# Kernel tuning notes

Hardware: AMD Instinct MI355X
Metric: run time of the kernel (lower is better)

## Reference

```python
import jax, jax.numpy as jnp
import numpy as np

# Model dims
D = 2048        # hidden_size
H = 16          # num_heads
KVH = 8         # num_key_value_heads
DH = 128        # head_dim
NUM_SLOTS = 16  # state-cache slots
B = 4           # prefill segments (regularized ragged batch)
L = 2048        # tokens per segment
T = B * L
C = 64          # GLA chunk size (fused_chunk_gla)
NEG = -1e30


def setup_inputs() -> dict:
    key = jax.random.key(0)
    k0, k1, k2, k3 = jax.random.split(key, 4)
    hidden_states = jax.random.normal(k0, (T, D), jnp.float32)
    W_qkv = jax.random.normal(k1, (D, (H + 2 * KVH) * DH), jnp.float32) * 0.02
    b_qkv = jnp.zeros(((H + 2 * KVH) * DH,), jnp.float32)
    kv_cache = jax.random.normal(k2, (NUM_SLOTS, H, DH, DH), jnp.float32) * 0.1
    state_indices = jax.random.randint(k3, (B,), 0, NUM_SLOTS, jnp.int32)
    return {"hidden_states": hidden_states, "W_qkv": W_qkv, "b_qkv": b_qkv,
            "kv_cache": kv_cache, "state_indices": state_indices}


def _to_chunks(x):
    # [T, H, d] -> [n_chunks, B, C, H, d]
    return x.reshape(B, L // C, C, H, DH).transpose(1, 0, 2, 3, 4)


def _gla_chunk_body(mask):
    def body(S, inp):
        # S: [B,H,dk,dv]; qc/kc/vc/gc: [B,C,H,d]
        qc, kc, vc, gc = inp
        Bc = jnp.cumsum(gc, axis=1)                       # inclusive log-decay within chunk
        # inter-chunk: initial state decayed by exp(Bc)
        o_inter = jnp.einsum('bchk,bhkv->bchv', qc * jnp.exp(Bc), S)
        # intra-chunk causal scores: A_ij = sum_d q_i,d * exp(B_i - B_j)_d * k_j,d, j<=i
        diff = Bc[:, :, None] - Bc[:, None, :]            # [B,Ci,Cj,H,dk], <=0 on lower tri
        diff = jnp.where(mask[None, :, :, None, None], diff, NEG)
        A = jnp.einsum('bihk,bijhk,bjhk->bijh', qc, jnp.exp(diff), kc)
        o = o_inter + jnp.einsum('bijh,bjhv->bihv', A, vc)
        # state update: S' = diag(exp(B_last)) S + sum_j (k_j exp(B_last - B_j)) v_j^T
        b_last = Bc[:, -1]                                # [B,H,dk]
        kg = kc * jnp.exp(b_last[:, None] - Bc)
        S_new = S * jnp.exp(b_last)[..., None] + jnp.einsum('bchk,bchv->bhkv', kg, vc)
        return S_new, o
    return jax.checkpoint(body)


def _forward(hidden_states, W_qkv, b_qkv, kv_cache, state_indices):
    qkv = hidden_states @ W_qkv + b_qkv
    q = qkv[:, :H * DH].reshape(T, H, DH)
    k = qkv[:, H * DH:(H + KVH) * DH].reshape(T, KVH, DH)
    v = qkv[:, (H + KVH) * DH:].reshape(T, KVH, DH)
    n_rep = H // KVH
    k = jnp.repeat(k, n_rep, axis=1)                      # repeat_kv (3D branch)
    v = jnp.repeat(v, n_rep, axis=1)
    q = jax.nn.relu(q) * DH ** -0.5                       # q_feature_map + fused_chunk_gla scale
    k = jnp.minimum(jax.nn.sigmoid(k), 0.95)              # sigmoid + clamp(max=clamp_max)
    g = jnp.log1p(-k)                                     # (1 - k).log()

    S0 = kv_cache[state_indices]                          # [B,H,dk,dv] per-slot initial states
    mask = jnp.tril(jnp.ones((C, C), bool))
    _, o = jax.lax.scan(_gla_chunk_body(mask), S0,
                        (_to_chunks(q), _to_chunks(k), _to_chunks(v), _to_chunks(g)))
    # [n_chunks,B,C,H,dv] -> per-segment concat [T, H*dv]
    return o.transpose(1, 0, 2, 3, 4).reshape(T, H * DH)


def reference(hidden_states, W_qkv, b_qkv, kv_cache, state_indices):
    return _forward(hidden_states, W_qkv, b_qkv, kv_cache, state_indices)
```

## Files before the change

### kernel.cpp

```cpp
#include <hip/hip_runtime.h>
#include <hip/hip_bf16.h>
#include <math.h>

#define RSQRT_DH 0.08838834764831845f

typedef __attribute__((ext_vector_type(8))) short short8;
typedef __attribute__((ext_vector_type(4))) float floatx4;

#define BAR() do { asm volatile("" ::: "memory"); __builtin_amdgcn_s_barrier(); asm volatile("" ::: "memory"); } while (0)

static __device__ __forceinline__ float bf2f(unsigned short u) {
  return __uint_as_float(((unsigned int)u) << 16);
}
static __device__ __forceinline__ unsigned short f2bf(float f) {
  unsigned int x = __float_as_uint(f);
  return (unsigned short)((x + 0x7fffu + ((x >> 16) & 1u)) >> 16);
}
static __device__ __forceinline__ ushort4 f4bf(float a, float b, float c, float d) {
  ushort4 r; r.x = f2bf(a); r.y = f2bf(b); r.z = f2bf(c); r.w = f2bf(d); return r;
}
static __device__ __forceinline__ short8 ld8u(const unsigned short* p) {
  short4 a = *(const short4*)p;
  short4 b = *(const short4*)(p + 4);
  short8 r;
  r[0] = a.x; r[1] = a.y; r[2] = a.z; r[3] = a.w;
  r[4] = b.x; r[5] = b.y; r[6] = b.z; r[7] = b.w;
  return r;
}

__launch_bounds__(256)
__global__ void k_cvt(const float* __restrict__ in, unsigned short* __restrict__ out, int n4) {
  int i = blockIdx.x * 256 + threadIdx.x;
  if (i >= n4) return;
  float4 v = ((const float4*)in)[i];
  ((ushort4*)out)[i] = f4bf(v.x, v.y, v.z, v.w);
}

__launch_bounds__(256)
__global__ void k_cvt_wt(const float* __restrict__ W, unsigned short* __restrict__ Wt) {
  __shared__ float tile[32][33];
  int t = threadIdx.x;
  int c = t & 31, r = t >> 5;
  int bx = blockIdx.x, by = blockIdx.y;
#pragma unroll
  for (int j = 0; j < 4; ++j)
    tile[r + j * 8][c] = W[(size_t)(by * 32 + r + j * 8) * 4096 + bx * 32 + c];
  __syncthreads();
#pragma unroll
  for (int j = 0; j < 4; ++j)
    Wt[(size_t)(bx * 32 + r + j * 8) * 2048 + by * 32 + c] = f2bf(tile[c][r + j * 8]);
}

__launch_bounds__(512, 2)
__global__ void k_gemm(const unsigned short* __restrict__ A,
                       const unsigned short* __restrict__ Bt,
                       const float* __restrict__ bias,
                       unsigned short* __restrict__ qb,
                       unsigned short* __restrict__ kb,
                       unsigned short* __restrict__ vb,
                       float* __restrict__ gf) {
  __shared__ unsigned short lds[65536];

  const int tid = threadIdx.x;
  const int w = tid >> 6, l = tid & 63;
  const int wm = w >> 2, wn = w & 3;
  const int lr = l & 15, quad = l >> 4;

  const int id = blockIdx.x;
  const int x = id & 7, loc = id >> 3;
  const int bm = (x >> 1) * 8 + (loc >> 3);
  const int bn = (x & 1) * 8 + (loc & 7);
  const int m0 = bm * 256, n0 = bn * 256;

  const int srow = tid >> 2;
  const int scol = (((tid & 3) ^ ((tid >> 3) & 3)) << 3);
  const unsigned short* agp = A + (size_t)(m0 + srow) * 2048 + scol;
  const unsigned short* bgp = Bt + (size_t)(n0 + srow) * 2048 + scol;
  unsigned short* ldsA_dst = lds + w * 512;
  unsigned short* ldsB_dst = lds + 8192 + w * 512;

  auto stageA = [&](int d, int u, int ktile) {
    __builtin_amdgcn_global_load_lds(
        (const __attribute__((address_space(1))) void*)(agp + (size_t)u * 262144 + (size_t)ktile * 32),
        (__attribute__((address_space(3))) void*)(ldsA_dst + d * 16384 + u * 4096),
        16, 0, 0);
  };
  auto stageB = [&](int d, int u, int ktile) {
    __builtin_amdgcn_global_load_lds(
        (const __attribute__((address_space(1))) void*)(bgp + (size_t)u * 262144 + (size_t)ktile * 32),
        (__attribute__((address_space(3))) void*)(ldsB_dst + d * 16384 + u * 4096),
        16, 0, 0);
  };

  const int kcol = ((quad ^ ((lr >> 1) & 3)) << 3);
  const int arow_base = (wm * 128 + lr) * 32 + kcol;
  const int brow_base = (wn * 64 + lr) * 32 + kcol;

  floatx4 acc[8][4] = {};

#pragma unroll
  for (int pt = 0; pt < 3; ++pt) {
    stageA(pt, 0, pt); stageA(pt, 1, pt);
    stageB(pt, 0, pt); stageB(pt, 1, pt);
  }

  for (int t = 0; t < 64; ++t) {
    const int d = t & 3;
    const unsigned short* Ab = lds + d * 16384;
    const unsigned short* Bb = Ab + 8192;
    const int t3 = t + 3;
    const int d3 = t3 & 3;

    if (t < 62)       asm volatile("s_waitcnt vmcnt(8)" ::: "memory");
    else if (t == 62) asm volatile("s_waitcnt vmcnt(4)" ::: "memory");
    else              asm volatile("s_waitcnt vmcnt(0)" ::: "memory");
    BAR();

    short8 af[4], bfr[4];
#pragma unroll
    for (int i = 0; i < 4; ++i) af[i] = *(const short8*)(Ab + arow_base + i * 512);
#pragma unroll
    for (int i = 0; i < 4; ++i) bfr[i] = *(const short8*)(Bb + brow_base + i * 512);
    if (t3 < 64) { stageA(d3, 0, t3); stageA(d3, 1, t3); }
    __builtin_amdgcn_s_setprio(1);
#pragma unroll
    for (int mi = 0; mi < 4; ++mi)
#pragma unroll
      for (int ni = 0; ni < 4; ++ni)
        acc[mi][ni] = __builtin_amdgcn_mfma_f32_16x16x32_bf16(af[mi], bfr[ni], acc[mi][ni], 0, 0, 0);
    __builtin_amdgcn_s_setprio(0);

    BAR();

#pragma unroll
    for (int i = 0; i < 4; ++i) af[i] = *(const short8*)(Ab + arow_base + 2048 + i * 512);
    if (t3 < 64) { stageB(d3, 0, t3); stageB(d3, 1, t3); }
    __builtin_amdgcn_s_setprio(1);
#pragma unroll
    for (int mi = 0; mi < 4; ++mi)
#pragma unroll
      for (int ni = 0; ni < 4; ++ni)
        acc[4 + mi][ni] = __builtin_amdgcn_mfma_f32_16x16x32_bf16(af[mi], bfr[ni], acc[4 + mi][ni], 0, 0, 0);
    __builtin_amdgcn_s_setprio(0);
  }

  float* ldsf = (float*)lds;
  __syncthreads();

  float4 bv;
  {
    const float* bp = bias + n0 + l * 4;
    bv.x = bp[0]; bv.y = bp[1]; bv.z = bp[2]; bv.w = bp[3];
  }

#pragma unroll
  for (int a = 0; a < 8; ++a) {
#pragma unroll
    for (int ni = 0; ni < 4; ++ni)
#pragma unroll
      for (int r = 0; r < 4; ++r)
        ldsf[(wm * 16 + quad * 4 + r) * 268 + wn * 64 + ni * 16 + lr] = acc[a][ni][r];
    __syncthreads();

    const int rbase = m0 + (a >> 2) * 64 + (a & 3) * 16;
#pragma unroll
    for (int it = 0; it < 4; ++it) {
      const int row32 = w * 4 + it;
      const int grow = rbase + (row32 >> 4) * 128 + (row32 & 15);
      float4 f = *(const float4*)&ldsf[row32 * 268 + l * 4];
      f.x += bv.x; f.y += bv.y; f.z += bv.z; f.w += bv.w;
      if (n0 < 2048) {
        *(ushort4*)(qb + (size_t)grow * 2048 + n0 + l * 4) =
            f4bf(fmaxf(f.x, 0.f) * RSQRT_DH, fmaxf(f.y, 0.f) * RSQRT_DH,
                 fmaxf(f.z, 0.f) * RSQRT_DH, fmaxf(f.w, 0.f) * RSQRT_DH);
      } else if (n0 < 3072) {
        float sx = fminf(1.f / (1.f + __expf(-f.x)), 0.95f);
        float sy = fminf(1.f / (1.f + __expf(-f.y)), 0.95f);
        float sz = fminf(1.f / (1.f + __expf(-f.z)), 0.95f);
        float sw = fminf(1.f / (1.f + __expf(-f.w)), 0.95f);
        size_t idx = (size_t)grow * 1024 + (n0 - 2048) + l * 4;
        *(ushort4*)(kb + idx) = f4bf(sx, sy, sz, sw);
        float4 g4; g4.x = log1pf(-sx); g4.y = log1pf(-sy);
        g4.z = log1pf(-sz); g4.w = log1pf(-sw);
        *(float4*)(gf + idx) = g4;
      } else {
        *(ushort4*)(vb + (size_t)grow * 1024 + (n0 - 3072) + l * 4) =
            f4bf(f.x, f.y, f.z, f.w);
      }
    }
    if (a < 7) __syncthreads();
  }
}

__launch_bounds__(256)
__global__ void k_phaseA(const unsigned short* __restrict__ kb,
                         const unsigned short* __restrict__ vb,
                         const float* __restrict__ gf,
                         float* __restrict__ blast,
                         unsigned short* __restrict__ Pb) {
  __shared__ float sBc[64 * 128];
  __shared__ float sKg[64 * 128];
  const int t = threadIdx.x;
  const int chunk = blockIdx.x, chain = blockIdx.y;
  const int b = chain >> 4, h = chain & 15, kvh = h >> 1;
  const int t0 = b * 2048 + chunk * 64;

#pragma unroll
  for (int rep = 0; rep < 8; ++rep) {
    int e = rep * 256 + t;
    int i = e >> 5, d4 = e & 31;
    *(float4*)(sBc + i * 128 + d4 * 4) =
        *(const float4*)(gf + (size_t)(t0 + i) * 1024 + kvh * 128 + d4 * 4);
  }
  __syncthreads();
  if (t < 128) {
    float run = sBc[t];
    for (int i = 1; i < 64; ++i) { run += sBc[i * 128 + t]; sBc[i * 128 + t] = run; }
    blast[((size_t)chain * 32 + chunk) * 128 + t] = run;
  }
  __syncthreads();
#pragma unroll
  for (int rep = 0; rep < 32; ++rep) {
    int e = rep * 256 + t;
    int i = e >> 7, d = e & 127;
    float kk = bf2f(kb[(size_t)(t0 + i) * 1024 + kvh * 128 + d]);
    sKg[e] = kk * __expf(sBc[63 * 128 + d] - sBc[e]);
  }
  __syncthreads();
  const int kq = t >> 3, vq = t & 7;
  const int kd0 = kq * 4, vd0 = vq * 16;
  float acc[4][16] = {};
  const unsigned short* vrow = vb + (size_t)t0 * 1024 + kvh * 128 + vd0;
  for (int i = 0; i < 64; ++i) {
    float4 kg4 = *(const float4*)(sKg + i * 128 + kd0);
    float ka[4] = {kg4.x, kg4.y, kg4.z, kg4.w};
    ushort4 v0 = *(const ushort4*)(vrow + (size_t)i * 1024);
    ushort4 v1 = *(const ushort4*)(vrow + (size_t)i * 1024 + 4);
    ushort4 v2 = *(const ushort4*)(vrow + (size_t)i * 1024 + 8);
    ushort4 v3 = *(const ushort4*)(vrow + (size_t)i * 1024 + 12);
    float vf[16] = {bf2f(v0.x), bf2f(v0.y), bf2f(v0.z), bf2f(v0.w),
                    bf2f(v1.x), bf2f(v1.y), bf2f(v1.z), bf2f(v1.w),
                    bf2f(v2.x), bf2f(v2.y), bf2f(v2.z), bf2f(v2.w),
                    bf2f(v3.x), bf2f(v3.y), bf2f(v3.z), bf2f(v3.w)};
#pragma unroll
    for (int r = 0; r < 4; ++r)
#pragma unroll
      for (int j = 0; j < 16; ++j) acc[r][j] += ka[r] * vf[j];
  }
  size_t pbase = ((size_t)chain * 32 + chunk) * 16384;
#pragma unroll
  for (int r = 0; r < 4; ++r)
#pragma unroll
    for (int j4 = 0; j4 < 4; ++j4)
      *(ushort4*)(Pb + pbase + (size_t)(kd0 + r) * 128 + vd0 + j4 * 4) =
          f4bf(acc[r][j4 * 4], acc[r][j4 * 4 + 1], acc[r][j4 * 4 + 2], acc[r][j4 * 4 + 3]);
}

__launch_bounds__(256)
__global__ void k_scan(const float* __restrict__ kv_cache,
                       const int* __restrict__ sidx,
                       const float* __restrict__ blast,
                       const unsigned short* __restrict__ Pb,
                       unsigned short* __restrict__ Sb) {
  const int t = threadIdx.x;
  const int part = blockIdx.x;
  const int chain = blockIdx.y;
  const int b = chain >> 4, h = chain & 15;
  const int e0 = part * 1024 + t * 4;
  const int kd = e0 >> 7;
  const int slot = sidx[b];
  float4 s = *(const float4*)(kv_cache + ((size_t)slot * 16 + h) * 16384 + e0);
#pragma unroll 1
  for (int c = 0; c < 32; ++c) {
    *(ushort4*)(Sb + ((size_t)c * 64 + chain) * 16384 + e0) = f4bf(s.x, s.y, s.z, s.w);
    float eb = __expf(blast[((size_t)chain * 32 + c) * 128 + kd]);
    ushort4 p = *(const ushort4*)(Pb + ((size_t)chain * 32 + c) * 16384 + e0);
    s.x = s.x * eb + bf2f(p.x);
    s.y = s.y * eb + bf2f(p.y);
    s.z = s.z * eb + bf2f(p.z);
    s.w = s.w * eb + bf2f(p.w);
  }
}

__launch_bounds__(256)
__global__ void k_output(const unsigned short* __restrict__ qb,
                         const unsigned short* __restrict__ kb,
                         const unsigned short* __restrict__ vb,
                         const float* __restrict__ gf,
                         const unsigned short* __restrict__ Sb,
                         float* __restrict__ out) {
  __shared__ float sBc[64 * 128];
  __shared__ unsigned short sR3[11136];
  unsigned short* sA   = sR3;
  unsigned short* sKE  = sR3 + 4608;
  unsigned short* sQE2 = sR3 + 4608 + 4352;
  unsigned short* sQE0 = sR3;
  unsigned short* sSt  = sR3 + 4608;
  unsigned short* sVt  = sR3 + 4608;

  const int t = threadIdx.x;
  const int w = t >> 6, l = t & 63;
  const int lr = l & 15, quad = l >> 4;
  const int chunk = blockIdx.x, chain = blockIdx.y;
  const int b = chain >> 4, h = chain & 15, kvh = h >> 1;
  const int t0 = b * 2048 + chunk * 64;
  const size_t sbase = ((size_t)chunk * 64 + chain) * 16384;

#pragma unroll
  for (int rep = 0; rep < 8; ++rep) {
    int e = rep * 256 + t, i = e >> 5, d4 = e & 31;
    *(float4*)(sBc + i * 128 + d4 * 4) =
        *(const float4*)(gf + (size_t)(t0 + i) * 1024 + kvh * 128 + d4 * 4);
  }
  __syncthreads();
  if (t < 128) {
    float run = sBc[t];
#pragma unroll
    for (int i = 1; i < 64; ++i) { run += sBc[i * 128 + t]; sBc[i * 128 + t] = run; }
  }

  floatx4 o[8];
#pragma unroll
  for (int i = 0; i < 8; ++i) o[i] = 0.f;

#pragma unroll
  for (int kh = 0; kh < 2; ++kh) {
    __syncthreads();
#pragma unroll
    for (int rep = 0; rep < 2; ++rep) {
      int idx = rep * 256 + t;
      int i = idx >> 3, g = idx & 7;
      int k0 = kh * 64 + g * 8;
      short8 q8 = *(const short8*)(qb + (size_t)(t0 + i) * 2048 + h * 128 + k0);
      short8 r;
#pragma unroll
      for (int u = 0; u < 8; ++u)
        r[u] = (short)f2bf(bf2f((unsigned short)q8[u]) * __expf(sBc[i * 128 + k0 + u]));
      *(short8*)(sQE0 + i * 72 + g * 8) = r;
    }
#pragma unroll
    for (int vh = 0; vh < 2; ++vh) {
      __syncthreads();
#pragma unroll
      for (int rep = 0; rep < 2; ++rep) {
        int idx = rep * 256 + t;
        int kl = idx >> 3, g = idx & 7;
        short8 s8 = *(const short8*)(Sb + sbase + (size_t)(kh * 64 + kl) * 128 + vh * 64 + g * 8);
#pragma unroll
        for (int u = 0; u < 8; ++u) sSt[(g * 8 + u) * 76 + kl] = (unsigned short)s8[u];
      }
      __syncthreads();
      short8 af0 = *(const short8*)(sQE0 + (w * 16 + lr) * 72 + quad * 8);
      short8 af1 = *(const short8*)(sQE0 + (w * 16 + lr) * 72 + 32 + quad * 8);
#pragma unroll
      for (int tv = 0; tv < 4; ++tv) {
        const unsigned short* bp = sSt + (tv * 16 + lr) * 76 + quad * 8;
        short8 bf0 = ld8u(bp);
        short8 bf1 = ld8u(bp + 32);
        o[vh * 4 + tv] = __builtin_amdgcn_mfma_f32_16x16x32_bf16(af0, bf0, o[vh * 4 + tv], 0, 0, 0);
        o[vh * 4 + tv] = __builtin_amdgcn_mfma_f32_16x16x32_bf16(af1, bf1, o[vh * 4 + tv], 0, 0, 0);
      }
    }
  }

  __syncthreads();
  for (int idx = t; idx < 576; idx += 256)
    *(short8*)(sA + idx * 8) = (short8)0;
#pragma unroll
  for (int I = 0; I < 4; ++I) {
    const float* Rrow = (I > 0) ? (sBc + (I * 16 - 1) * 128) : nullptr;
    for (int base = 0; base < (I + 1) * 16; base += 32) {
      int nrows = min(32, (I + 1) * 16 - base);
      __syncthreads();
      int ngroups = nrows * 16;
      for (int idx = t; idx < ngroups; idx += 256) {
        int jl = idx >> 4, g = idx & 15;
        int j = base + jl, k0 = g * 8;
        short8 k8 = *(const short8*)(kb + (size_t)(t0 + j) * 1024 + kvh * 128 + k0);
        short8 r;
#pragma unroll
        for (int u = 0; u < 8; ++u) {
          int k = k0 + u;
          float Rk = Rrow ? Rrow[k] : 0.f;
          r[u] = (short)f2bf(bf2f((unsigned short)k8[u]) * __expf(Rk - sBc[j * 128 + k]));
        }
        *(short8*)(sKE + jl * 136 + k0) = r;
      }
      if (base == 0) {
        {
          int idx = t;
          int il = idx >> 4, g = idx & 15;
          int i = I * 16 + il, k0 = g * 8;
          short8 q8 = *(const short8*)(qb + (size_t)(t0 + i) * 2048 + h * 128 + k0);
          short8 r;
#pragma unroll
          for (int u = 0; u < 8; ++u) {
            int k = k0 + u;
            float Rk = Rrow ? Rrow[k] : 0.f;
            r[u] = (short)f2bf(bf2f((unsigned short)q8[u]) * __expf(sBc[i * 128 + k] - Rk));
          }
          *(short8*)(sQE2 + il * 136 + k0) = r;
        }
      }
      __syncthreads();
      const int J = w;
      if (J * 16 >= base && J * 16 < base + nrows) {
        floatx4 a4 = {};
#pragma unroll
        for (int ks = 0; ks < 4; ++ks) {
          short8 afr = *(const short8*)(sQE2 + lr * 136 + ks * 32 + quad * 8);
          short8 bfr = *(const short8*)(sKE + (J * 16 - base + lr) * 136 + ks * 32 + quad * 8);
          a4 = __builtin_amdgcn_mfma_f32_16x16x32_bf16(afr, bfr, a4, 0, 0, 0);
        }
#pragma unroll
        for (int r = 0; r < 4; ++r) {
          int il = quad * 4 + r;
          float v = ((J < I) || (lr <= il)) ? a4[r] : 0.f;
          sA[(I * 16 + il) * 72 + J * 16 + lr] = f2bf(v);
        }
      }
    }
  }

  __syncthreads();
  short8 aA0 = *(const short8*)(sA + (w * 16 + lr) * 72 + quad * 8);
  short8 aA1 = *(const short8*)(sA + (w * 16 + lr) * 72 + 32 + quad * 8);
#pragma unroll
  for (int vh = 0; vh < 2; ++vh) {
    if (vh) __syncthreads();
#pragma unroll
    for (int rep = 0; rep < 2; ++rep) {
      int idx = rep * 256 + t;
      int j = idx >> 3, g = idx & 7;
      short8 v8 = *(const short8*)(vb + (size_t)(t0 + j) * 1024 + kvh * 128 + vh * 64 + g * 8);
#pragma unroll
      for (int u = 0; u < 8; ++u) sVt[(g * 8 + u) * 76 + j] = (unsigned short)v8[u];
    }
    __syncthreads();
#pragma unroll
    for (int tv = 0; tv < 4; ++tv) {
      const unsigned short* bp = sVt + (tv * 16 + lr) * 76 + quad * 8;
      short8 b0 = ld8u(bp);
      short8 b1 = ld8u(bp + 32);
      o[vh * 4 + tv] = __builtin_amdgcn_mfma_f32_16x16x32_bf16(aA0, b0, o[vh * 4 + tv], 0, 0, 0);
      o[vh * 4 + tv] = __builtin_amdgcn_mfma_f32_16x16x32_bf16(aA1, b1, o[vh * 4 + tv], 0, 0, 0);
    }
  }

#pragma unroll
  for (int tv8 = 0; tv8 < 8; ++tv8) {
    int col = (tv8 >> 2) * 64 + (tv8 & 3) * 16 + lr;
#pragma unroll
    for (int r = 0; r < 4; ++r) {
      int i = w * 16 + quad * 4 + r;
      out[(size_t)(t0 + i) * 2048 + h * 128 + col] = o[tv8][r];
    }
  }
}

extern "C" void kernel_launch(void* const* d_in, const int* in_sizes, int n_in,
                              void* d_out, int out_size, void* d_ws, size_t ws_size,
                              hipStream_t stream) {
  (void)in_sizes; (void)n_in; (void)out_size; (void)ws_size;
  const float* hs   = (const float*)d_in[0];
  const float* W    = (const float*)d_in[1];
  const float* bias = (const float*)d_in[2];
  const float* kvc  = (const float*)d_in[3];
  const int*   sidx = (const int*)d_in[4];

  char* ws = (char*)d_ws;
  unsigned short* Sb  = (unsigned short*)(ws + 0);
  unsigned short* hsb = (unsigned short*)(ws + 0);
  unsigned short* wtb = (unsigned short*)(ws + 33554432);
  unsigned short* qb  = (unsigned short*)(ws + 67108864);
  unsigned short* kb  = (unsigned short*)(ws + 100663296);
  unsigned short* vb  = (unsigned short*)(ws + 117440512);
  float*          gf  = (float*)(ws + 134217728);
  float*          bl  = (float*)(ws + 167772160);
  unsigned short* Pb  = (unsigned short*)d_out;
  float* out = (float*)d_out;

  k_cvt<<<dim3(16384), dim3(256), 0, stream>>>(hs, hsb, 16777216 / 4);
  k_cvt_wt<<<dim3(128, 64), dim3(256), 0, stream>>>(W, wtb);
  k_gemm<<<dim3(512), dim3(512), 0, stream>>>(hsb, wtb, bias, qb, kb, vb, gf);
  k_phaseA<<<dim3(32, 64), dim3(256), 0, stream>>>(kb, vb, gf, bl, Pb);
  k_scan<<<dim3(16, 64), dim3(256), 0, stream>>>(kvc, sidx, bl, Pb, Sb);
  k_output<<<dim3(32, 64), dim3(256), 0, stream>>>(qb, kb, vb, gf, Sb, out);
}
```

Measured before the change: 588.9 us.

## Restructure QKV GEMM to double-buffered K=64 tiles and parallelize chunk cumsum

The QKV projection GEMM main loop moves from a 4-stage ring of K=32 tiles to a 2-stage double buffer of K=64 tiles with a new XOR swizzle. Each K tile is split into four MFMA quadrants, with fragment loads and global-to-LDS prefetch interleaved between barriers, so there are fewer loop iterations and more MFMA work per synchronization. Separately, the per-chunk cumulative sum in phaseA and the output kernel becomes a log-step parallel scan over all 256 threads instead of a serial 64-step loop on 128 threads. The tradeoffs are a shallower prefetch depth in the GEMM, more barriers per iteration, and extra LDS traffic and barriers in the scan.

```diff
diff --git a/kernel.cpp b/kernel.cpp
--- a/kernel.cpp
+++ b/kernel.cpp
@@ -8,6 +8,7 @@
 typedef __attribute__((ext_vector_type(4))) float floatx4;
 
 #define BAR() do { asm volatile("" ::: "memory"); __builtin_amdgcn_s_barrier(); asm volatile("" ::: "memory"); } while (0)
+#define MFMA16(a, b, c) __builtin_amdgcn_mfma_f32_16x16x32_bf16((a), (b), (c), 0, 0, 0)
 
 static __device__ __forceinline__ float bf2f(unsigned short u) {
   return __uint_as_float(((unsigned int)u) << 16);
@@ -60,6 +61,7 @@
                        unsigned short* __restrict__ vb,
                        float* __restrict__ gf) {
   __shared__ unsigned short lds[65536];
+  char* lb = (char*)lds;
 
   const int tid = threadIdx.x;
   const int w = tid >> 6, l = tid & 63;
@@ -72,76 +74,118 @@
   const int bn = (x & 1) * 8 + (loc & 7);
   const int m0 = bm * 256, n0 = bn * 256;
 
-  const int srow = tid >> 2;
-  const int scol = (((tid & 3) ^ ((tid >> 3) & 3)) << 3);
-  const unsigned short* agp = A + (size_t)(m0 + srow) * 2048 + scol;
-  const unsigned short* bgp = Bt + (size_t)(n0 + srow) * 2048 + scol;
-  unsigned short* ldsA_dst = lds + w * 512;
-  unsigned short* ldsB_dst = lds + 8192 + w * 512;
-
-  auto stageA = [&](int d, int u, int ktile) {
+  const int srow = tid >> 3;
+  const int sslot = (tid & 7) ^ (srow & 7);
+  const unsigned short* agp = A + (size_t)(m0 + srow) * 2048 + sslot * 8;
+  const unsigned short* bgp = Bt + (size_t)(n0 + srow) * 2048 + sslot * 8;
+
+  auto stA = [&](int d, int h, int s, int kt) {
     __builtin_amdgcn_global_load_lds(
-        (const __attribute__((address_space(1))) void*)(agp + (size_t)u * 262144 + (size_t)ktile * 32),
-        (__attribute__((address_space(3))) void*)(ldsA_dst + d * 16384 + u * 4096),
+        (const __attribute__((address_space(1))) void*)(agp + (size_t)(h * 128 + s * 64) * 2048 + kt * 64),
+        (__attribute__((address_space(3))) void*)(lb + d * 65536 + h * 16384 + s * 8192 + tid * 16),
         16, 0, 0);
   };
-  auto stageB = [&](int d, int u, int ktile) {
+  auto stB = [&](int d, int h, int s, int kt) {
     __builtin_amdgcn_global_load_lds(
-        (const __attribute__((address_space(1))) void*)(bgp + (size_t)u * 262144 + (size_t)ktile * 32),
-        (__attribute__((address_space(3))) void*)(ldsB_dst + d * 16384 + u * 4096),
+        (const __attribute__((address_space(1))) void*)(bgp + (size_t)(h * 128 + s * 64) * 2048 + kt * 64),
+        (__attribute__((address_space(3))) void*)(lb + d * 65536 + 32768 + h * 16384 + s * 8192 + tid * 16),
         16, 0, 0);
   };
 
-  const int kcol = ((quad ^ ((lr >> 1) & 3)) << 3);
-  const int arow_base = (wm * 128 + lr) * 32 + kcol;
-  const int brow_base = (wn * 64 + lr) * 32 + kcol;
+  const int c16_0 = ((quad) ^ (lr & 7)) * 16;
+  const int c16_1 = ((4 + quad) ^ (lr & 7)) * 16;
+  const char* pAb = lb + wm * 16384 + lr * 128;
+  const char* pBb = lb + 32768 + (wn >> 1) * 16384 + ((wn & 1) * 64 + lr) * 128;
 
   floatx4 acc[8][4] = {};
-
-#pragma unroll
-  for (int pt = 0; pt < 3; ++pt) {
-    stageA(pt, 0, pt); stageA(pt, 1, pt);
-    stageB(pt, 0, pt); stageB(pt, 1, pt);
-  }
-
-  for (int t = 0; t < 64; ++t) {
-    const int d = t & 3;
-    const unsigned short* Ab = lds + d * 16384;
-    const unsigned short* Bb = Ab + 8192;
-    const int t3 = t + 3;
-    const int d3 = t3 & 3;
-
-    if (t < 62)       asm volatile("s_waitcnt vmcnt(8)" ::: "memory");
-    else if (t == 62) asm volatile("s_waitcnt vmcnt(4)" ::: "memory");
-    else              asm volatile("s_waitcnt vmcnt(0)" ::: "memory");
-    BAR();
-
-    short8 af[4], bfr[4];
-#pragma unroll
-    for (int i = 0; i < 4; ++i) af[i] = *(const short8*)(Ab + arow_base + i * 512);
-#pragma unroll
-    for (int i = 0; i < 4; ++i) bfr[i] = *(const short8*)(Bb + brow_base + i * 512);
-    if (t3 < 64) { stageA(d3, 0, t3); stageA(d3, 1, t3); }
+  short8 fa[4][2], fb0[2][2], fb1[2][2];
+
+  stA(0, 0, 0, 0); stA(0, 0, 1, 0); stA(0, 1, 0, 0); stA(0, 1, 1, 0);
+  stB(0, 0, 0, 0); stB(0, 0, 1, 0); stB(0, 1, 0, 0); stB(0, 1, 1, 0);
+  asm volatile("s_waitcnt vmcnt(0)" ::: "memory");
+  BAR();
+
+  for (int t = 0; t < 32; ++t) {
+    const int d = t & 1, dn = d ^ 1;
+    const char* pA = pAb + d * 65536;
+    const char* pB = pBb + d * 65536;
+    const bool st = (t < 31);
+    const int kt1 = t + 1;
+
+#pragma unroll
+    for (int mi = 0; mi < 4; ++mi) {
+      fa[mi][0] = *(const short8*)(pA + (mi * 16) * 128 + c16_0);
+      fa[mi][1] = *(const short8*)(pA + (mi * 16) * 128 + c16_1);
+    }
+#pragma unroll
+    for (int ni = 0; ni < 2; ++ni) {
+      fb0[ni][0] = *(const short8*)(pB + (ni * 16) * 128 + c16_0);
+      fb0[ni][1] = *(const short8*)(pB + (ni * 16) * 128 + c16_1);
+    }
+    if (st) { stA(dn, 0, 0, kt1); stA(dn, 0, 1, kt1); stA(dn, 1, 0, kt1); stA(dn, 1, 1, kt1); }
+    BAR();
+    asm volatile("s_waitcnt lgkmcnt(0)" ::: "memory");
     __builtin_amdgcn_s_setprio(1);
 #pragma unroll
     for (int mi = 0; mi < 4; ++mi)
 #pragma unroll
-      for (int ni = 0; ni < 4; ++ni)
-        acc[mi][ni] = __builtin_amdgcn_mfma_f32_16x16x32_bf16(af[mi], bfr[ni], acc[mi][ni], 0, 0, 0);
+      for (int ni = 0; ni < 2; ++ni) {
+        acc[mi][ni] = MFMA16(fa[mi][0], fb0[ni][0], acc[mi][ni]);
+        acc[mi][ni] = MFMA16(fa[mi][1], fb0[ni][1], acc[mi][ni]);
+      }
     __builtin_amdgcn_s_setprio(0);
-
-    BAR();
-
-#pragma unroll
-    for (int i = 0; i < 4; ++i) af[i] = *(const short8*)(Ab + arow_base + 2048 + i * 512);
-    if (t3 < 64) { stageB(d3, 0, t3); stageB(d3, 1, t3); }
+    BAR();
+
+#pragma unroll
+    for (int ni = 0; ni < 2; ++ni) {
+      fb1[ni][0] = *(const short8*)(pB + (32 + ni * 16) * 128 + c16_0);
+      fb1[ni][1] = *(const short8*)(pB + (32 + ni * 16) * 128 + c16_1);
+    }
+    if (st) { stB(dn, 0, 0, kt1); stB(dn, 0, 1, kt1); stB(dn, 1, 0, kt1); stB(dn, 1, 1, kt1); }
+    BAR();
+    asm volatile("s_waitcnt lgkmcnt(0)" ::: "memory");
     __builtin_amdgcn_s_setprio(1);
 #pragma unroll
     for (int mi = 0; mi < 4; ++mi)
 #pragma unroll
-      for (int ni = 0; ni < 4; ++ni)
-        acc[4 + mi][ni] = __builtin_amdgcn_mfma_f32_16x16x32_bf16(af[mi], bfr[ni], acc[4 + mi][ni], 0, 0, 0);
+      for (int ni = 0; ni < 2; ++ni) {
+        acc[mi][2 + ni] = MFMA16(fa[mi][0], fb1[ni][0], acc[mi][2 + ni]);
+        acc[mi][2 + ni] = MFMA16(fa[mi][1], fb1[ni][1], acc[mi][2 + ni]);
+      }
     __builtin_amdgcn_s_setprio(0);
+    BAR();
+
+#pragma unroll
+    for (int mi = 0; mi < 4; ++mi) {
+      fa[mi][0] = *(const short8*)(pA + (64 + mi * 16) * 128 + c16_0);
+      fa[mi][1] = *(const short8*)(pA + (64 + mi * 16) * 128 + c16_1);
+    }
+    if (st) asm volatile("s_waitcnt vmcnt(4)" ::: "memory");
+    BAR();
+    asm volatile("s_waitcnt lgkmcnt(0)" ::: "memory");
+    __builtin_amdgcn_s_setprio(1);
+#pragma unroll
+    for (int mi = 0; mi < 4; ++mi)
+#pragma unroll
+      for (int ni = 0; ni < 2; ++ni) {
+        acc[4 + mi][2 + ni] = MFMA16(fa[mi][0], fb1[ni][0], acc[4 + mi][2 + ni]);
+        acc[4 + mi][2 + ni] = MFMA16(fa[mi][1], fb1[ni][1], acc[4 + mi][2 + ni]);
+      }
+    __builtin_amdgcn_s_setprio(0);
+    BAR();
+
+    if (st) asm volatile("s_waitcnt vmcnt(0)" ::: "memory");
+    BAR();
+    __builtin_amdgcn_s_setprio(1);
+#pragma unroll
+    for (int mi = 0; mi < 4; ++mi)
+#pragma unroll
+      for (int ni = 0; ni < 2; ++ni) {
+        acc[4 + mi][ni] = MFMA16(fa[mi][0], fb0[ni][0], acc[4 + mi][ni]);
+        acc[4 + mi][ni] = MFMA16(fa[mi][1], fb0[ni][1], acc[4 + mi][ni]);
+      }
+    __builtin_amdgcn_s_setprio(0);
+    BAR();
   }
 
   float* ldsf = (float*)lds;
@@ -192,6 +236,32 @@
   }
 }
 
+static __device__ __forceinline__ void scan64x128(float* sBc, int t) {
+  float4* x4 = (float4*)sBc;
+#pragma unroll
+  for (int s = 1; s < 64; s <<= 1) {
+    const int off = s * 32;
+    float4 a[8];
+#pragma unroll
+    for (int j = 0; j < 8; ++j) {
+      int e = j * 256 + t;
+      if (e >= off) {
+        float4 cu = x4[e];
+        float4 pr = x4[e - off];
+        a[j].x = cu.x + pr.x; a[j].y = cu.y + pr.y;
+        a[j].z = cu.z + pr.z; a[j].w = cu.w + pr.w;
+      }
+    }
+    __syncthreads();
+#pragma unroll
+    for (int j = 0; j < 8; ++j) {
+      int e = j * 256 + t;
+      if (e >= off) x4[e] = a[j];
+    }
+    __syncthreads();
+  }
+}
+
 __launch_bounds__(256)
 __global__ void k_phaseA(const unsigned short* __restrict__ kb,
                          const unsigned short* __restrict__ vb,
@@ -213,12 +283,8 @@
         *(const float4*)(gf + (size_t)(t0 + i) * 1024 + kvh * 128 + d4 * 4);
   }
   __syncthreads();
-  if (t < 128) {
-    float run = sBc[t];
-    for (int i = 1; i < 64; ++i) { run += sBc[i * 128 + t]; sBc[i * 128 + t] = run; }
-    blast[((size_t)chain * 32 + chunk) * 128 + t] = run;
-  }
-  __syncthreads();
+  scan64x128(sBc, t);
+  if (t < 128) blast[((size_t)chain * 32 + chunk) * 128 + t] = sBc[63 * 128 + t];
 #pragma unroll
   for (int rep = 0; rep < 32; ++rep) {
     int e = rep * 256 + t;
@@ -313,11 +379,7 @@
         *(const float4*)(gf + (size_t)(t0 + i) * 1024 + kvh * 128 + d4 * 4);
   }
   __syncthreads();
-  if (t < 128) {
-    float run = sBc[t];
-#pragma unroll
-    for (int i = 1; i < 64; ++i) { run += sBc[i * 128 + t]; sBc[i * 128 + t] = run; }
-  }
+  scan64x128(sBc, t);
 
   floatx4 o[8];
 #pragma unroll
@@ -357,8 +419,8 @@
         const unsigned short* bp = sSt + (tv * 16 + lr) * 76 + quad * 8;
         short8 bf0 = ld8u(bp);
         short8 bf1 = ld8u(bp + 32);
-        o[vh * 4 + tv] = __builtin_amdgcn_mfma_f32_16x16x32_bf16(af0, bf0, o[vh * 4 + tv], 0, 0, 0);
-        o[vh * 4 + tv] = __builtin_amdgcn_mfma_f32_16x16x32_bf16(af1, bf1, o[vh * 4 + tv], 0, 0, 0);
+        o[vh * 4 + tv] = MFMA16(af0, bf0, o[vh * 4 + tv]);
+        o[vh * 4 + tv] = MFMA16(af1, bf1, o[vh * 4 + tv]);
       }
     }
   }
@@ -410,7 +472,7 @@
         for (int ks = 0; ks < 4; ++ks) {
           short8 afr = *(const short8*)(sQE2 + lr * 136 + ks * 32 + quad * 8);
           short8 bfr = *(const short8*)(sKE + (J * 16 - base + lr) * 136 + ks * 32 + quad * 8);
-          a4 = __builtin_amdgcn_mfma_f32_16x16x32_bf16(afr, bfr, a4, 0, 0, 0);
+          a4 = MFMA16(afr, bfr, a4);
         }
 #pragma unroll
         for (int r = 0; r < 4; ++r) {
@@ -442,8 +504,8 @@
       const unsigned short* bp = sVt + (tv * 16 + lr) * 76 + quad * 8;
       short8 b0 = ld8u(bp);
       short8 b1 = ld8u(bp + 32);
-      o[vh * 4 + tv] = __builtin_amdgcn_mfma_f32_16x16x32_bf16(aA0, b0, o[vh * 4 + tv], 0, 0, 0);
-      o[vh * 4 + tv] = __builtin_amdgcn_mfma_f32_16x16x32_bf16(aA1, b1, o[vh * 4 + tv], 0, 0, 0);
+      o[vh * 4 + tv] = MFMA16(aA0, b0, o[vh * 4 + tv]);
+      o[vh * 4 + tv] = MFMA16(aA1, b1, o[vh * 4 + tv]);
     }
   }
 
```

Measured after the change: 606.3 us. +3.0%, slower.
